# Performance work log

Hardware: AMD Instinct MI355X
Metric: run time of the kernel (lower is better)

## Reference

```python
import jax, jax.numpy as jnp
import numpy as np

NEG = -100000.0
V, E, HID, K = 30000, 256, 512, 32   # vocab, embed_dim, hidden_size, tag_size
H = HID // 2                          # per-direction LSTM hidden
B, T = 128, 512                       # batch, seq_len
START, END = K - 2, K - 1


def setup_inputs() -> dict:
    keys = iter(jax.random.split(jax.random.key(0), 40))

    def u(shape, scale):
        return jax.random.uniform(next(keys), shape, jnp.float32, -scale, scale)

    inp = {}
    inp["words"] = jax.random.randint(next(keys), (B, T), 0, V)
    inp["labels"] = jax.random.randint(next(keys), (B, T), 0, K - 2)
    inp["emb"] = jax.random.normal(next(keys), (V, E), jnp.float32)
    s = 1.0 / float(np.sqrt(H))
    for l, din in [(0, E), (1, HID)]:
        for d in ("f", "b"):
            inp[f"Wih{l}{d}"] = u((4 * H, din), s)
            inp[f"Whh{l}{d}"] = u((4 * H, H), s)
            inp[f"b{l}{d}"] = u((4 * H,), s)
    st = 1.0 / float(np.sqrt(HID))
    inp["Wtag"] = u((K, HID), st)
    inp["btag"] = u((K,), st)
    tm = u((K, K), float(np.sqrt(3.0 / K)))  # kaiming-uniform-like
    inp["trans"] = tm.at[START, :].set(NEG).at[:, END].set(NEG)
    return inp


def _lstm_dir(x, Wih, Whh, b, reverse):
    # x: [T, B, Din] seq-major; standard torch LSTM cell, gate order i,f,g,o
    Hd = Whh.shape[1]
    z = jnp.zeros((x.shape[1], Hd), x.dtype)

    def step(carry, xt):
        h, c = carry
        g = xt @ Wih.T + h @ Whh.T + b
        i, f, gg, o = jnp.split(g, 4, axis=-1)
        c = jax.nn.sigmoid(f) * c + jax.nn.sigmoid(i) * jnp.tanh(gg)
        h = jax.nn.sigmoid(o) * jnp.tanh(c)
        return (h, c), h

    _, hs = jax.lax.scan(step, (z, z), x, reverse=reverse)
    return hs  # [T, B, Hd], aligned with x even when reverse=True


def reference(words, labels, emb, Wih0f, Whh0f, b0f, Wih0b, Whh0b, b0b,
              Wih1f, Whh1f, b1f, Wih1b, Whh1b, b1b, Wtag, btag, trans):
    x = emb[words].transpose(1, 0, 2)  # [T, B, E]
    h1 = jnp.concatenate([_lstm_dir(x, Wih0f, Whh0f, b0f, False),
                          _lstm_dir(x, Wih0b, Whh0b, b0b, True)], axis=-1)
    h2 = jnp.concatenate([_lstm_dir(h1, Wih1f, Whh1f, b1f, False),
                          _lstm_dir(h1, Wih1b, Whh1b, b1b, True)], axis=-1)
    emit = h2 @ Wtag.T + btag          # [T, B, K]
    lab = labels.T                     # [T, B]
    Bn = lab.shape[1]

    # ---- gold path score ----
    prev = jnp.concatenate([jnp.full((1, Bn), START, lab.dtype), lab], axis=0)
    cur = jnp.concatenate([lab, jnp.full((1, Bn), END, lab.dtype)], axis=0)
    gold_trans = trans[cur, prev].sum(axis=0)                                   # [B]
    gold_emit = jnp.take_along_axis(emit, lab[:, :, None], axis=-1)[..., 0].sum(axis=0)
    gold = gold_trans + gold_emit

    # ---- log partition (forward algorithm) ----
    dp0 = jnp.full((Bn, K), NEG, emit.dtype).at[:, START].set(0.0)

    def part_step(dp, e_t):
        cur_logit = trans[None] + e_t[:, :, None] + dp[:, None, :]  # [B, K_cur, K_prev]
        return jax.nn.logsumexp(cur_logit, axis=-1), None

    dp, _ = jax.lax.scan(part_step, dp0, emit)
    logZ = jax.nn.logsumexp(dp + trans[END][None, :], axis=-1)
    nll = jnp.mean(logZ - gold)

    # ---- viterbi (max-plus DP + backtrace) ----
    def vit_step(dp_v, e_t):
        cur_score = trans[None] + e_t[:, :, None] + dp_v[:, None, :]
        return cur_score.max(axis=-1), cur_score.argmax(axis=-1)

    dpv, bps = jax.lax.scan(vit_step, dp0, emit)   # bps: [T, B, K]
    dpv = dpv + trans[END][None, :]
    best = dpv.argmax(axis=-1)                      # [B]

    def back(tag, bp_t):
        prev_tag = jnp.take_along_axis(bp_t, tag[:, None], axis=1)[:, 0]
        return prev_tag, tag

    _, path = jax.lax.scan(back, best, bps, reverse=True)  # [T, B]
    return nll, path.T
```

## Files before the change

### kernel.cpp

```cpp
#include <hip/hip_runtime.h>
#include <math.h>

#define T_LEN 512
#define BATCH 128
#define KTAG  32
#define START_TAG 30
#define END_TAG   31
#define NEGV  -100000.0f

#define L2E    1.4426950408889634f
#define TWOL2E 2.8853900817779268f
#define LN2    0.6931471805599453f

typedef __attribute__((ext_vector_type(4))) short bf16x4;
typedef __attribute__((ext_vector_type(8))) short bf16x8;
typedef __attribute__((ext_vector_type(4))) float f32x4;
#define MFMA16   __builtin_amdgcn_mfma_f32_16x16x32_bf16
#define MFMA16F8 __builtin_amdgcn_mfma_f32_16x16x32_fp8_fp8
#define EXP2(x)  __builtin_amdgcn_exp2f(x)
#define RCP(x)   __builtin_amdgcn_rcpf(x)

__device__ __forceinline__ short f2bf(float x) {
    unsigned int u = __float_as_uint(x);
    u += 0x7fffu + ((u >> 16) & 1u);
    return (short)(u >> 16);
}

__device__ __forceinline__ f32x4 bf4_to_f32x4(bf16x4 v) {
    union { bf16x4 s; uint2 u; } c; c.s = v;
    f32x4 r;
    r[0] = __uint_as_float(c.u.x << 16);
    r[1] = __uint_as_float(c.u.x & 0xffff0000u);
    r[2] = __uint_as_float(c.u.y << 16);
    r[3] = __uint_as_float(c.u.y & 0xffff0000u);
    return r;
}

__device__ __forceinline__ unsigned char f2fp8(float x) {
    unsigned u = __float_as_uint(x);
    unsigned s = (u >> 24) & 0x80u;
    unsigned mag = u & 0x7fffffffu;
    if (mag >= 0x43e80000u) return (unsigned char)(s | 0x7e);
    int e = (int)(mag >> 23) - 127;
    int ulp_exp = (e < -6) ? -9 : (e - 3);
    float C = __uint_as_float((unsigned)((ulp_exp + 23 + 127) << 23)) * 1.5f;
    float r = (__uint_as_float(mag) + C) - C;
    unsigned ru = __float_as_uint(r);
    int re = (int)(ru >> 23) - 127;
    unsigned code;
    if (r == 0.0f) code = 0;
    else if (re < -6) code = (unsigned)(r * 512.0f);
    else code = (unsigned)((re + 7) << 3) | ((ru >> 20) & 7u);
    return (unsigned char)(s | code);
}

__device__ __forceinline__ unsigned pack2_fp8(float h0, float h1) {
#if __has_builtin(__builtin_amdgcn_cvt_pk_fp8_f32)
    return (unsigned)__builtin_amdgcn_cvt_pk_fp8_f32(h0, h1, 0, false);
#else
    return (unsigned)f2fp8(h0) | ((unsigned)f2fp8(h1) << 8);
#endif
}

__global__ void fill_kernel(float* out, int n, float v) {
    int i = blockIdx.x * 256 + threadIdx.x;
    if (i < n) out[i] = v;
}

__device__ __forceinline__ void dev_pack_bf16(const float* __restrict__ W,
                                              short* __restrict__ out, int K, int idx) {
    const int KT = K >> 5;
    int i  = idx & 7;
    int ln = (idx >> 3) & 63;
    int rem = idx >> 9;
    int kt = rem % KT;
    int wt = rem / KT;
    int type = wt & 3, w = wt >> 2;
    int row = type * 256 + w * 16 + (ln & 15);
    int col = kt * 32 + ((ln >> 4) << 3) + i;
    float sc = (type == 2) ? TWOL2E : L2E;
    out[idx] = f2bf(W[(size_t)row * K + col] * sc);
}

__device__ __forceinline__ void dev_pack_fp8(const float* __restrict__ W,
                                             unsigned char* __restrict__ out, int K, int idx) {
    const int KT = K >> 5;
    int i  = idx & 7;
    int ln = (idx >> 3) & 63;
    int rem = idx >> 9;
    int kt = rem % KT;
    int wt = rem / KT;
    int type = wt & 3, w = wt >> 2;
    int row = type * 256 + w * 16 + (ln & 15);
    int col = kt * 32 + ((ln >> 4) << 3) + i;
    float sc = (type == 2) ? TWOL2E : L2E;
    out[idx] = f2fp8(W[(size_t)row * K + col] * sc);
}

__device__ __forceinline__ void dev_pack_wtag(const float* __restrict__ Wtag,
                                              unsigned char* __restrict__ out, int idx) {
    int i  = idx & 7;
    int ln = (idx >> 3) & 63;
    int kt = (idx >> 9) & 7;
    int nt = (idx >> 12) & 1;
    int dir = idx >> 13;
    int row = nt * 16 + (ln & 15);
    int col = dir * 256 + kt * 32 + ((ln >> 4) << 3) + i;
    out[idx] = f2fp8(Wtag[row * 512 + col]);
}

__global__ __launch_bounds__(256) void pack_all(
    const float* Wih0f, const float* Wih0b, const float* Wih1f, const float* Wih1b,
    const float* Whh0f, const float* Whh0b, const float* Whh1f, const float* Whh1b,
    const float* Wtag, const float* emb,
    short* wq0f, short* wq0b, short* wq1f, short* wq1b,
    unsigned char* h80f, unsigned char* h80b, unsigned char* h81f, unsigned char* h81b,
    unsigned char* wtag8, short* embq)
{
    const int bx = blockIdx.x;
    const int tid = threadIdx.x;
    if (bx < 2048) {
        const float* W = (bx < 1024) ? Wih0f : Wih0b;
        short* o = (bx < 1024) ? wq0f : wq0b;
        dev_pack_bf16(W, o, 256, (bx & 1023) * 256 + tid);
    } else if (bx < 6144) {
        const float* W = (bx < 4096) ? Wih1f : Wih1b;
        short* o = (bx < 4096) ? wq1f : wq1b;
        dev_pack_bf16(W, o, 512, ((bx - 2048) & 2047) * 256 + tid);
    } else if (bx < 10240) {
        int seg = (bx - 6144) >> 10;
        const float* W = (seg == 0) ? Whh0f : (seg == 1) ? Whh0b : (seg == 2) ? Whh1f : Whh1b;
        unsigned char* o = (seg == 0) ? h80f : (seg == 1) ? h80b : (seg == 2) ? h81f : h81b;
        dev_pack_fp8(W, o, 256, ((bx - 6144) & 1023) * 256 + tid);
    } else if (bx < 10304) {
        dev_pack_wtag(Wtag, wtag8, (bx - 10240) * 256 + tid);
    } else {
        int i = (bx - 10304) * 256 + tid;
        embq[i] = f2bf(emb[i]);
    }
}

template <int LAYER, int AMODE>
__device__ __forceinline__ void gemm_role(
    int gb, int C, const int* __restrict__ words, const void* __restrict__ Asrc,
    const short* __restrict__ BfF, const short* __restrict__ BfB,
    const float* __restrict__ bsF, const float* __restrict__ bsB,
    short* __restrict__ preF, short* __restrict__ preB, int s0, char* smraw)
{
    constexpr int K  = (LAYER == 0) ? 256 : 512;
    constexpr int KT = K / 32;
    constexpr int RB = K * 2;
    constexpr int NT = (LAYER == 0) ? 2 : 1;
    constexpr int NH = 4 / NT;

    const int dir = gb / (NH * C);
    int rem = gb - dir * NH * C;
    const int half = rem / C;
    const int gx = rem - half * C;
    const int sblk = gx >> 3, bg = gx & 7;
    const int t0 = half * NT;
    const int tid = threadIdx.x;
    const int wv = tid >> 6, L = tid & 63;
    const int wid = wv;
    const int brow = L & 15, kgrp = L >> 4;

    const short* Bf = dir ? BfB : BfF;
    const float* bias = dir ? bsB : bsF;
    short* pre = dir ? preB : preF;
    short* As = (short*)smraw;

    const bf16x8* Bp = (const bf16x8*)Bf;
    bf16x8 bw[NT][KT];
#pragma unroll
    for (int u = 0; u < NT; ++u)
#pragma unroll
        for (int kt = 0; kt < KT; ++kt)
            bw[u][kt] = Bp[(((wid * 4 + t0 + u) * KT + kt) << 6) + L];

    float bb[NT];
#pragma unroll
    for (int u = 0; u < NT; ++u) {
        float sc = ((t0 + u) == 2) ? TWOL2E : L2E;
        bb[u] = bias[(t0 + u) * 256 + wid * 16 + brow] * sc;
    }

    for (int sl = 0; sl < 8; ++sl) {
        const int sloc = sblk * 8 + sl;
        const int t = dir ? (T_LEN - 1 - (s0 + sloc)) : (s0 + sloc);

        {
            char* lds = (char*)As;
            if (LAYER == 0) {
                if (tid < 512) {
                    const int row = tid >> 5, ch = tid & 31;
                    const int b = bg * 16 + row;
                    const int cb = ch * 16;
                    const int word = words[b * T_LEN + t];
                    if (AMODE == 0) {
                        const char* src = (const char*)Asrc + (size_t)word * 512 + cb;
                        *(bf16x8*)(lds + ((row * RB + cb) ^ ((row & 7) << 4))) = *(const bf16x8*)src;
                    } else {
                        const float* src = (const float*)Asrc + (size_t)word * 256 + ch * 8;
                        float4 f0 = *(const float4*)(src);
                        float4 f1 = *(const float4*)(src + 4);
                        short tmp[8] = {f2bf(f0.x), f2bf(f0.y), f2bf(f0.z), f2bf(f0.w),
                                        f2bf(f1.x), f2bf(f1.y), f2bf(f1.z), f2bf(f1.w)};
                        *(bf16x8*)(lds + ((row * RB + cb) ^ ((row & 7) << 4))) = *(const bf16x8*)tmp;
                    }
                }
            } else {
                const int row = tid >> 6, ch = tid & 63;
                const int b = bg * 16 + row;
                const int cb = ch * 16;
                const char* src = (const char*)Asrc + ((size_t)t * BATCH + b) * 1024 + cb;
                *(bf16x8*)(lds + ((row * RB + cb) ^ ((row & 7) << 4))) = *(const bf16x8*)src;
            }
        }
        __syncthreads();

        f32x4 acc[NT];
#pragma unroll
        for (int u = 0; u < NT; ++u) acc[u] = (f32x4){bb[u], bb[u], bb[u], bb[u]};

        const char* lds = (const char*)As;
#pragma unroll
        for (int kt = 0; kt < KT; ++kt) {
            bf16x8 a = *(const bf16x8*)(lds + ((brow * RB + kt * 64 + kgrp * 16) ^ ((brow & 7) << 4)));
#pragma unroll
            for (int u = 0; u < NT; ++u)
                acc[u] = MFMA16(a, bw[u][kt], acc[u], 0, 0, 0);
        }

        bf16x4* pp = (bf16x4*)pre;
        const size_t base = ((((size_t)sloc * 8 + bg) * 16 + wid) * 4 + t0) * 64 + L;
#pragma unroll
        for (int u = 0; u < NT; ++u) {
            bf16x4 o = {f2bf(acc[u][0]), f2bf(acc[u][1]), f2bf(acc[u][2]), f2bf(acc[u][3])};
            pp[base + (size_t)u * 64] = o;
        }
        __syncthreads();
    }
}

__global__ __launch_bounds__(1024) void gemm_only0(
    const int* words, const void* Asrc, const short* BfF, const short* BfB,
    const float* bsF, const float* bsB, short* preF, short* preB, int s0, int C, int amode)
{
    constexpr int SMB = 8192;
    __shared__ __align__(16) char smraw[SMB];
    if (amode == 0)
        gemm_role<0, 0>(blockIdx.x, C, words, Asrc, BfF, BfB, bsF, bsB, preF, preB, s0, smraw);
    else
        gemm_role<0, 1>(blockIdx.x, C, words, Asrc, BfF, BfB, bsF, bsB, preF, preB, s0, smraw);
}

__global__ __launch_bounds__(1024) void gemm_only1(
    const int* words, const void* Asrc, const short* BfF, const short* BfB,
    const float* bsF, const float* bsB, short* preF, short* preB, int s0, int C)
{
    constexpr int SMB = 16384;
    __shared__ __align__(16) char smraw[SMB];
    gemm_role<1, 2>(blockIdx.x, C, words, Asrc, BfF, BfB, bsF, bsB, preF, preB, s0, smraw);
}

template <int LAYER, int AMODE>
__global__ __launch_bounds__(1024) void fused_chunk(
    const int* __restrict__ words, const void* __restrict__ xsrc,
    const short* __restrict__ wihF, const short* __restrict__ wihB,
    const float* __restrict__ biasF, const float* __restrict__ biasB,
    short* __restrict__ preOutF, short* __restrict__ preOutB, int s0g, int gemm_on,
    const short* __restrict__ preF, const short* __restrict__ preB,
    const unsigned char* __restrict__ whhF, const unsigned char* __restrict__ whhB,
    short* __restrict__ h1out,
    const unsigned char* __restrict__ wtagf, const float* __restrict__ btag,
    float* __restrict__ emitF, float* __restrict__ emitB,
    float* __restrict__ stC, long* __restrict__ stH,
    int s0, int C)
{
    constexpr int SMB = (LAYER == 1) ? (8704 + 32768) : 8704;
    __shared__ __align__(16) char smraw[SMB];

    if (blockIdx.x >= 32) {
        if (gemm_on)
            gemm_role<LAYER, AMODE>(blockIdx.x - 32, C, words, xsrc, wihF, wihB,
                                    biasF, biasB, preOutF, preOutB, s0g, smraw);
        return;
    }

    const int dir  = blockIdx.x >> 4;
    const int bg   = (blockIdx.x >> 1) & 7;
    const int half = blockIdx.x & 1;
    const int tid = threadIdx.x;
    const int wid = tid >> 6;
    const int L   = tid & 63;
    const int brow = L & 15;
    const int kgrp = L >> 4;
    const int Lp = (L + half * 32) & 63;

    const bf16x4* pre = (const bf16x4*)(dir ? preB : preF);
    long* hb0 = (long*)smraw;
    long* hb1 = (long*)(smraw + 4352);
    float (*ep)[8][16][32] = (float(*)[8][16][32])(smraw + 8704);

    const long* Wp = (const long*)(dir ? whhB : whhF);
    long whh[32];
#pragma unroll
    for (int tt = 0; tt < 4; ++tt)
#pragma unroll
        for (int kt = 0; kt < 8; ++kt)
            whh[tt * 8 + kt] = Wp[(((wid * 4 + tt) * 8 + kt) << 6) + L];

    long wt0 = 0, wt1 = 0;
    if (LAYER == 1) {
        int kw = (wid < 8) ? wid : 7;
        const long* wtp = (const long*)wtagf;
        wt0 = wtp[(((dir * 2 + 0) * 8 + kw) << 6) + L];
        wt1 = wtp[(((dir * 2 + 1) * 8 + kw) << 6) + L];
    }

    float cs0, cs1;
    if (s0 == 0) {
        for (int q = tid; q < 544; q += 1024) hb0[q] = 0;
        cs0 = cs1 = 0.f;
    } else {
        for (int q = tid; q < 544; q += 1024)
            hb0[q] = stH[(size_t)blockIdx.x * 544 + q];
        float2 c2 = ((const float2*)stC)[blockIdx.x * 1024 + tid];
        cs0 = c2.x; cs1 = c2.y;
    }
    for (int q = tid; q < 544; q += 1024) hb1[q] = 0;
    __syncthreads();

    const size_t pstride = 8 * 16 * 4 * 64;
    const size_t pbase = (((size_t)bg * 16 + wid) * 4) * 64 + Lp;
    bf16x4 pc0 = pre[pbase + 0 * 64];
    bf16x4 pc1 = pre[pbase + 1 * 64];
    bf16x4 pc2 = pre[pbase + 2 * 64];
    bf16x4 pc3 = pre[pbase + 3 * 64];

    const int srcL = L & 31;
    const bool lo = (L < 32);
    const int rb = ((srcL >> 4) << 2) + (lo ? 0 : 2);
    const int jj = wid * 16 + (L & 15);

    for (int s = s0; s < s0 + C; ++s) {
        const int sloc = s - s0;
        const int par = s & 1;
        const char* ldsr = (const char*)(par ? hb1 : hb0);
        char* ldsw = (char*)(par ? hb0 : hb1);

        f32x4 acc0 = bf4_to_f32x4(pc0);
        f32x4 acc1 = bf4_to_f32x4(pc1);
        f32x4 acc2 = bf4_to_f32x4(pc2);
        f32x4 acc3 = bf4_to_f32x4(pc3);

        {
            const int sl2 = (sloc + 1 < C) ? sloc + 1 : sloc;
            const size_t pb = (size_t)sl2 * pstride + pbase;
            pc0 = pre[pb + 0 * 64];
            pc1 = pre[pb + 1 * 64];
            pc2 = pre[pb + 2 * 64];
            pc3 = pre[pb + 3 * 64];
        }

#pragma unroll
        for (int kt = 0; kt < 8; ++kt) {
            long a = *(const long*)(ldsr + brow * 272 + kt * 32 + kgrp * 8);
            acc0 = MFMA16F8(a, whh[0 * 8 + kt], acc0, 0, 0, 0);
            acc1 = MFMA16F8(a, whh[1 * 8 + kt], acc1, 0, 0, 0);
            acc2 = MFMA16F8(a, whh[2 * 8 + kt], acc2, 0, 0, 0);
            acc3 = MFMA16F8(a, whh[3 * 8 + kt], acc3, 0, 0, 0);
        }

        if (LAYER == 1 && sloc >= 1 && wid < 8) {
            long a = *(const long*)(ldsr + brow * 272 + wid * 32 + kgrp * 8);
            f32x4 e0 = {0.f, 0.f, 0.f, 0.f}, e1 = {0.f, 0.f, 0.f, 0.f};
            e0 = MFMA16F8(a, wt0, e0, 0, 0, 0);
            e1 = MFMA16F8(a, wt1, e1, 0, 0, 0);
#pragma unroll
            for (int r = 0; r < 4; ++r) {
                int bl = (kgrp << 2) + r;
                ep[par][wid][bl][brow] = e0[r];
                ep[par][wid][bl][16 + brow] = e1[r];
            }
        }

        if (LAYER == 1 && sloc >= 2 && tid < 256) {
            int bl = tid >> 5, tg = tid & 31;
            float v = 0.f;
#pragma unroll
            for (int p = 0; p < 8; ++p) v += ep[par ^ 1][p][bl][tg];
            const int x = s - 2;
            const int tp = dir ? (T_LEN - 1 - x) : x;
            size_t ei = ((size_t)tp * BATCH + bg * 16 + half * 8 + bl) * KTAG + tg;
            if (dir == 0) emitF[ei] = v + btag[tg];
            else          emitB[ei] = v;
        }

        float g0v0, g0v1, g1v0, g1v1, g2v0, g2v1, g3v0, g3v1;
        {
            float a00 = __shfl(acc0[2], srcL), a01 = __shfl(acc0[3], srcL);
            float a10 = __shfl(acc1[2], srcL), a11 = __shfl(acc1[3], srcL);
            float a20 = __shfl(acc2[2], srcL), a21 = __shfl(acc2[3], srcL);
            float a30 = __shfl(acc3[2], srcL), a31 = __shfl(acc3[3], srcL);
            g0v0 = lo ? acc0[0] : a00;  g0v1 = lo ? acc0[1] : a01;
            g1v0 = lo ? acc1[0] : a10;  g1v1 = lo ? acc1[1] : a11;
            g2v0 = lo ? acc2[0] : a20;  g2v1 = lo ? acc2[1] : a21;
            g3v0 = lo ? acc3[0] : a30;  g3v1 = lo ? acc3[1] : a31;
        }

        float hh0, hh1;
        {
            float ig, fg, gg, og;
            ig = RCP(1.0f + EXP2(-g0v0)); fg = RCP(1.0f + EXP2(-g1v0));
            gg = 1.0f - 2.0f * RCP(1.0f + EXP2(g2v0));
            og = RCP(1.0f + EXP2(-g3v0));
            cs0 = fg * cs0 + ig * gg;
            hh0 = og * (1.0f - 2.0f * RCP(1.0f + EXP2(TWOL2E * cs0)));
            ig = RCP(1.0f + EXP2(-g0v1)); fg = RCP(1.0f + EXP2(-g1v1));
            gg = 1.0f - 2.0f * RCP(1.0f + EXP2(g2v1));
            og = RCP(1.0f + EXP2(-g3v1));
            cs1 = fg * cs1 + ig * gg;
            hh1 = og * (1.0f - 2.0f * RCP(1.0f + EXP2(TWOL2E * cs1)));
        }

        {
            unsigned pk = pack2_fp8(hh0, hh1);
            ldsw[(rb + 0) * 272 + jj] = (char)(pk);
            ldsw[(rb + 1) * 272 + jj] = (char)(pk >> 8);
            if (LAYER == 0) {
                const int t = dir ? (T_LEN - 1 - s) : s;
                size_t gb = ((size_t)t * BATCH + bg * 16 + half * 8 + rb) * 512 + dir * 256 + jj;
                h1out[gb]       = f2bf(hh0);
                h1out[gb + 512] = f2bf(hh1);
            }
        }
        __syncthreads();
    }

    if (LAYER == 1) {
        if (wid < 8) {
            const char* ldsr = (const char*)hb0;
            long a = *(const long*)(ldsr + brow * 272 + wid * 32 + kgrp * 8);
            f32x4 e0 = {0.f, 0.f, 0.f, 0.f}, e1 = {0.f, 0.f, 0.f, 0.f};
            e0 = MFMA16F8(a, wt0, e0, 0, 0, 0);
            e1 = MFMA16F8(a, wt1, e1, 0, 0, 0);
#pragma unroll
            for (int r = 0; r < 4; ++r) {
                int bl = (kgrp << 2) + r;
                ep[0][wid][bl][brow] = e0[r];
                ep[0][wid][bl][16 + brow] = e1[r];
            }
        }
        if (tid < 256) {
            int bl = tid >> 5, tg = tid & 31;
            float v = 0.f;
#pragma unroll
            for (int p = 0; p < 8; ++p) v += ep[1][p][bl][tg];
            const int x = s0 + C - 2;
            const int tp = dir ? (T_LEN - 1 - x) : x;
            size_t ei = ((size_t)tp * BATCH + bg * 16 + half * 8 + bl) * KTAG + tg;
            if (dir == 0) emitF[ei] = v + btag[tg];
            else          emitB[ei] = v;
        }
        __syncthreads();
        if (tid < 256) {
            int bl = tid >> 5, tg = tid & 31;
            float v = 0.f;
#pragma unroll
            for (int p = 0; p < 8; ++p) v += ep[0][p][bl][tg];
            const int x = s0 + C - 1;
            const int tp = dir ? (T_LEN - 1 - x) : x;
            size_t ei = ((size_t)tp * BATCH + bg * 16 + half * 8 + bl) * KTAG + tg;
            if (dir == 0) emitF[ei] = v + btag[tg];
            else          emitB[ei] = v;
        }
    }

    for (int q = tid; q < 544; q += 1024)
        stH[(size_t)blockIdx.x * 544 + q] = hb0[q];
    ((float2*)stC)[blockIdx.x * 1024 + tid] = (float2){cs0, cs1};
}

__global__ __launch_bounds__(64) void crf_half(
    const float* __restrict__ emitF, const float* __restrict__ emitB,
    const float* __restrict__ trans,
    float* __restrict__ alph, float* __restrict__ betap,
    float* __restrict__ alphV, float* __restrict__ betaV,
    unsigned char* __restrict__ bpsW, unsigned char* __restrict__ npsW)
{
    const int lane = threadIdx.x;
    const int k = lane & 31;
    const int h = lane >> 5;
    const int p0 = h << 4;
    const int role = blockIdx.x >> 7;
    const int b = blockIdx.x & 127;

    __shared__ unsigned char ptr_l[256 * KTAG];

    if (role == 0) {
        float trow2[16];
#pragma unroll
        for (int i = 0; i < 4; ++i) {
            float4 f = *(const float4*)(trans + k * KTAG + p0 + i * 4);
            trow2[i * 4 + 0] = f.x * L2E; trow2[i * 4 + 1] = f.y * L2E;
            trow2[i * 4 + 2] = f.z * L2E; trow2[i * 4 + 3] = f.w * L2E;
        }
        float dp = (k == START_TAG) ? 0.0f : NEGV * L2E;
        size_t e0i = (size_t)b * KTAG + k;
        float e2 = (emitF[e0i] + emitB[e0i]) * L2E;

        for (int t = 0; t < 256; ++t) {
            float e_next2 = 0.0f;
            if (t + 1 < 256) {
                size_t ei = ((size_t)(t + 1) * BATCH + b) * KTAG + k;
                e_next2 = (emitF[ei] + emitB[ei]) * L2E;
            }
            float v[16];
#pragma unroll
            for (int q = 0; q < 16; ++q)
                v[q] = trow2[q] + __shfl(dp, p0 + q);
            float mx[8];
#pragma unroll
            for (int i = 0; i < 8; ++i) mx[i] = fmaxf(v[i], v[i + 8]);
#pragma unroll
            for (int i = 0; i < 4; ++i) mx[i] = fmaxf(mx[i], mx[i + 4]);
            float halfm = fmaxf(fmaxf(mx[0], mx[1]), fmaxf(mx[2], mx[3]));
            float m = fmaxf(halfm, __shfl_xor(halfm, 32));
            float es[16];
#pragma unroll
            for (int i = 0; i < 16; ++i) es[i] = EXP2(v[i] - m);
#pragma unroll
            for (int i = 0; i < 8; ++i) es[i] += es[i + 8];
#pragma unroll
            for (int i = 0; i < 4; ++i) es[i] += es[i + 4];
            float shalf = (es[0] + es[1]) + (es[2] + es[3]);
            float ssum = shalf + __shfl_xor(shalf, 32);
            dp = e2 + m + __log2f(ssum);
            e2 = e_next2;
        }
        if (lane < 32) alph[b * KTAG + k] = dp;
    } else if (role == 1) {
        float trowT2[16];
#pragma unroll
        for (int i = 0; i < 16; ++i)
            trowT2[i] = trans[(p0 + i) * KTAG + k] * L2E;
        float beta = trans[END_TAG * KTAG + k] * L2E;
        size_t e0i = ((size_t)511 * BATCH + b) * KTAG + k;
        float e2 = (emitF[e0i] + emitB[e0i]) * L2E;

        for (int it = 0; it < 256; ++it) {
            const int t = 510 - it;
            float e_next2 = 0.0f;
            if (it + 1 < 256) {
                size_t ei = ((size_t)t * BATCH + b) * KTAG + k;
                e_next2 = (emitF[ei] + emitB[ei]) * L2E;
            }
            float z = beta + e2;
            float v[16];
#pragma unroll
            for (int q = 0; q < 16; ++q)
                v[q] = trowT2[q] + __shfl(z, p0 + q);
            float mx[8];
#pragma unroll
            for (int i = 0; i < 8; ++i) mx[i] = fmaxf(v[i], v[i + 8]);
#pragma unroll
            for (int i = 0; i < 4; ++i) mx[i] = fmaxf(mx[i], mx[i + 4]);
            float halfm = fmaxf(fmaxf(mx[0], mx[1]), fmaxf(mx[2], mx[3]));
            float m = fmaxf(halfm, __shfl_xor(halfm, 32));
            float es[16];
#pragma unroll
            for (int i = 0; i < 16; ++i) es[i] = EXP2(v[i] - m);
#pragma unroll
            for (int i = 0; i < 8; ++i) es[i] += es[i + 8];
#pragma unroll
            for (int i = 0; i < 4; ++i) es[i] += es[i + 4];
            float shalf = (es[0] + es[1]) + (es[2] + es[3]);
            float ssum = shalf + __shfl_xor(shalf, 32);
            beta = m + __log2f(ssum);
            e2 = e_next2;
        }
        if (lane < 32) betap[b * KTAG + k] = beta;
    } else if (role == 2) {
        float trow[16];
#pragma unroll
        for (int i = 0; i < 4; ++i) {
            float4 f = *(const float4*)(trans + k * KTAG + p0 + i * 4);
            trow[i * 4 + 0] = f.x; trow[i * 4 + 1] = f.y;
            trow[i * 4 + 2] = f.z; trow[i * 4 + 3] = f.w;
        }
        float dpv = (k == START_TAG) ? 0.0f : NEGV;
        size_t e0i = (size_t)b * KTAG + k;
        float e = emitF[e0i] + emitB[e0i];

        for (int t = 0; t < 256; ++t) {
            float e_next = 0.0f;
            if (t + 1 < 256) {
                size_t ei = ((size_t)(t + 1) * BATCH + b) * KTAG + k;
                e_next = emitF[ei] + emitB[ei];
            }
            float w[16];
#pragma unroll
            for (int q = 0; q < 16; ++q)
                w[q] = trow[q] + __shfl(dpv, p0 + q);
            float bv_[8]; int bi_[8];
#pragma unroll
            for (int i = 0; i < 8; ++i) {
                bool g = w[2 * i + 1] > w[2 * i];
                bv_[i] = g ? w[2 * i + 1] : w[2 * i];
                bi_[i] = p0 + (g ? 2 * i + 1 : 2 * i);
            }
#pragma unroll
            for (int i = 0; i < 4; ++i) {
                bool g = bv_[2 * i + 1] > bv_[2 * i];
                bv_[i] = g ? bv_[2 * i + 1] : bv_[2 * i];
                bi_[i] = g ? bi_[2 * i + 1] : bi_[2 * i];
            }
            { bool g = bv_[3] > bv_[2]; bv_[1] = g ? bv_[3] : bv_[2]; bi_[1] = g ? bi_[3] : bi_[2]; }
            { bool g = bv_[1] > bv_[0]; bv_[0] = g ? bv_[1] : bv_[0]; bi_[0] = g ? bi_[1] : bi_[0]; }
            float ov = __shfl_xor(bv_[0], 32);
            int   oi = __shfl_xor(bi_[0], 32);
            bool g2 = h ? (ov >= bv_[0]) : (ov > bv_[0]);
            float bm  = g2 ? ov : bv_[0];
            int  barg = g2 ? oi : bi_[0];
            dpv = e + bm;
            if (!h) ptr_l[t * KTAG + k] = (unsigned char)barg;
            e = e_next;
        }
        if (lane < 32) alphV[b * KTAG + k] = dpv;
        for (int i = lane; i < 2048; i += 64)
            ((unsigned*)bpsW)[(size_t)b * 2048 + i] = ((const unsigned*)ptr_l)[i];
    } else {
        float trowT[16];
#pragma unroll
        for (int i = 0; i < 16; ++i)
            trowT[i] = trans[(p0 + i) * KTAG + k];
        float bvv = trans[END_TAG * KTAG + k];
        size_t e0i = ((size_t)511 * BATCH + b) * KTAG + k;
        float e = emitF[e0i] + emitB[e0i];

        for (int it = 0; it < 256; ++it) {
            const int t = 510 - it;
            float e_next = 0.0f;
            if (it + 1 < 256) {
                size_t ei = ((size_t)t * BATCH + b) * KTAG + k;
                e_next = emitF[ei] + emitB[ei];
            }
            float z = bvv + e;
            float w[16];
#pragma unroll
            for (int q = 0; q < 16; ++q)
                w[q] = trowT[q] + __shfl(z, p0 + q);
            float bv_[8]; int bi_[8];
#pragma unroll
            for (int i = 0; i < 8; ++i) {
                bool g = w[2 * i + 1] > w[2 * i];
                bv_[i] = g ? w[2 * i + 1] : w[2 * i];
                bi_[i] = p0 + (g ? 2 * i + 1 : 2 * i);
            }
#pragma unroll
            for (int i = 0; i < 4; ++i) {
                bool g = bv_[2 * i + 1] > bv_[2 * i];
                bv_[i] = g ? bv_[2 * i + 1] : bv_[2 * i];
                bi_[i] = g ? bi_[2 * i + 1] : bi_[2 * i];
            }
            { bool g = bv_[3] > bv_[2]; bv_[1] = g ? bv_[3] : bv_[2]; bi_[1] = g ? bi_[3] : bi_[2]; }
            { bool g = bv_[1] > bv_[0]; bv_[0] = g ? bv_[1] : bv_[0]; bi_[0] = g ? bi_[1] : bi_[0]; }
            float ov = __shfl_xor(bv_[0], 32);
            int   oi = __shfl_xor(bi_[0], 32);
            bool g2 = h ? (ov >= bv_[0]) : (ov > bv_[0]);
            float bm  = g2 ? ov : bv_[0];
            int  barg = g2 ? oi : bi_[0];
            bvv = bm;
            if (!h) ptr_l[(t - 255) * KTAG + k] = (unsigned char)barg;
            e = e_next;
        }
        if (lane < 32) betaV[b * KTAG + k] = bvv;
        for (int i = lane; i < 2048; i += 64)
            ((unsigned*)npsW)[(size_t)b * 2048 + i] = ((const unsigned*)ptr_l)[i];
    }
}

__global__ __launch_bounds__(64) void crf_join(
    const float* __restrict__ emitF, const float* __restrict__ emitB,
    const float* __restrict__ trans, const int* __restrict__ labels,
    const float* __restrict__ alph, const float* __restrict__ betap,
    const float* __restrict__ alphV, const float* __restrict__ betaV,
    const unsigned char* __restrict__ bpsW, const unsigned char* __restrict__ npsW,
    float* __restrict__ diff, float* __restrict__ path_out)
{
    const int b = blockIdx.x;
    const int lane = threadIdx.x;
    const int k = lane & 31;

    __shared__ unsigned char bps_l[256 * KTAG];
    __shared__ unsigned char nps_l[256 * KTAG];
    __shared__ unsigned char pth[T_LEN];

    for (int i = lane; i < 2048; i += 64) {
        ((unsigned*)bps_l)[i] = ((const unsigned*)bpsW)[(size_t)b * 2048 + i];
        ((unsigned*)nps_l)[i] = ((const unsigned*)npsW)[(size_t)b * 2048 + i];
    }

    float fv = alph[b * KTAG + k] + betap[b * KTAG + k];
    float mm = fv;
    for (int off = 16; off; off >>= 1) mm = fmaxf(mm, __shfl_xor(mm, off));
    float contrib = (lane < KTAG) ? EXP2(fv - mm) : 0.0f;
    float ss = contrib;
    for (int off = 32; off; off >>= 1) ss += __shfl_xor(ss, off);
    float logZ = (mm + __log2f(ss)) * LN2;

    float gsum = 0.0f;
    for (int t = lane; t < T_LEN; t += 64) {
        int curl = labels[b * T_LEN + t];
        int prev = (t > 0) ? labels[b * T_LEN + t - 1] : START_TAG;
        size_t gi = ((size_t)t * BATCH + b) * KTAG + curl;
        gsum += trans[curl * KTAG + prev] + emitF[gi] + emitB[gi];
    }
    if (lane == 0) gsum += trans[END_TAG * KTAG + labels[b * T_LEN + T_LEN - 1]];
    for (int off = 32; off; off >>= 1) gsum += __shfl_xor(gsum, off);

    float av = alphV[b * KTAG + k] + betaV[b * KTAG + k];
    int bi = k;
    for (int off = 16; off; off >>= 1) {
        float ovv = __shfl_xor(av, off);
        int   oii = __shfl_xor(bi, off);
        if (ovv > av || (ovv == av && oii < bi)) { av = ovv; bi = oii; }
    }

    __syncthreads();
    if (lane == 0) {
        diff[b] = logZ - gsum;
        int pb = bi, pf = bi;
        pth[255] = (unsigned char)bi;
        for (int i = 1; i <= 256; ++i) {
            if (i <= 255) {
                pb = bps_l[(256 - i) * KTAG + pb];
                pth[255 - i] = (unsigned char)pb;
            }
            pf = nps_l[(i - 1) * KTAG + pf];
            pth[255 + i] = (unsigned char)pf;
        }
    }
    __syncthreads();
    for (int t = lane; t < T_LEN; t += 64)
        path_out[(size_t)b * T_LEN + t] = (float)pth[t];
}

__global__ void nll_kernel(const float* __restrict__ diff, float* __restrict__ out) {
    int lane = threadIdx.x;
    float v = diff[lane];
    __shared__ float red[2];
    for (int off = 32; off; off >>= 1) v += __shfl_xor(v, off);
    if ((lane & 63) == 0) red[lane >> 6] = v;
    __syncthreads();
    if (lane == 0) out[0] = (red[0] + red[1]) / 128.0f;
}

extern "C" void kernel_launch(void* const* d_in, const int* in_sizes, int n_in,
                              void* d_out, int out_size, void* d_ws, size_t ws_size,
                              hipStream_t stream) {
    (void)in_sizes; (void)n_in;

    const int*   words  = (const int*)d_in[0];
    const int*   labels = (const int*)d_in[1];
    const float* emb    = (const float*)d_in[2];
    const float* Wih0f  = (const float*)d_in[3];
    const float* Whh0f  = (const float*)d_in[4];
    const float* b0f    = (const float*)d_in[5];
    const float* Wih0b  = (const float*)d_in[6];
    const float* Whh0b  = (const float*)d_in[7];
    const float* b0b    = (const float*)d_in[8];
    const float* Wih1f  = (const float*)d_in[9];
    const float* Whh1f  = (const float*)d_in[10];
    const float* b1f    = (const float*)d_in[11];
    const float* Wih1b  = (const float*)d_in[12];
    const float* Whh1b  = (const float*)d_in[13];
    const float* b1b    = (const float*)d_in[14];
    const float* Wtag   = (const float*)d_in[15];
    const float* btag   = (const float*)d_in[16];
    const float* trans  = (const float*)d_in[17];
    float* out = (float*)d_out;
    char* ws = (char*)d_ws;

    const size_t WIH0B = (size_t)1024 * 256 * 2;
    const size_t WIH1B = (size_t)1024 * 512 * 2;
    const size_t WHH8B = (size_t)1024 * 256;
    const size_t WTAG8 = (size_t)16384;
    const size_t H1B   = (size_t)T_LEN * BATCH * 512 * 2;
    const size_t EMITB = (size_t)T_LEN * BATCH * KTAG * 4;
    const size_t EMBQB = (size_t)30000 * 256 * 2;
    const size_t STHB  = (size_t)32 * 544 * 8;
    const size_t STCB  = (size_t)32 * 1024 * 8;
    const size_t PSTEP = (size_t)BATCH * 1024 * 2;
    const size_t CRFAB = (size_t)4 * 128 * 32 * 4;
    const size_t BPSB  = (size_t)128 * 256 * 32;

    const size_t base0 = 2 * WIH0B + 2 * WIH1B + 4 * WHH8B + WTAG8 + H1B +
                         2 * EMITB + STHB + STCB + CRFAB + 2 * BPSB +
                         4096 + (1u << 20);

    int C = 0, use_embq = 0;
    for (int eq = 1; eq >= 0 && !C; --eq)
        for (int c = 256; c >= 16 && !C; c >>= 1)
            if (base0 + (eq ? EMBQB : 0) + 4 * (size_t)c * PSTEP <= ws_size) {
                C = c; use_embq = eq;
            }
    if (!C) {
        fill_kernel<<<(out_size + 255) / 256, 256, 0, stream>>>(
            out, out_size, (float)(ws_size >> 20));
        return;
    }

    size_t off = 0;
    auto alloc = [&](size_t bytes) -> char* {
        char* p = ws + off;
        off = (off + bytes + 255) & ~(size_t)255;
        return p;
    };
    short* wihq0f = (short*)alloc(WIH0B);
    short* wihq0b = (short*)alloc(WIH0B);
    short* wihq1f = (short*)alloc(WIH1B);
    short* wihq1b = (short*)alloc(WIH1B);
    unsigned char* whh8_0f = (unsigned char*)alloc(WHH8B);
    unsigned char* whh8_0b = (unsigned char*)alloc(WHH8B);
    unsigned char* whh8_1f = (unsigned char*)alloc(WHH8B);
    unsigned char* whh8_1b = (unsigned char*)alloc(WHH8B);
    unsigned char* wtag8   = (unsigned char*)alloc(WTAG8);
    short* h1     = (short*)alloc(H1B);
    float* emF    = (float*)alloc(EMITB);
    float* emB    = (float*)alloc(EMITB);
    long*  stH    = (long*)alloc(STHB);
    float* stC    = (float*)alloc(STCB);
    float* diff   = (float*)alloc(4096);
    float* crfa   = (float*)alloc(CRFAB);
    unsigned char* bpsW = (unsigned char*)alloc(BPSB);
    unsigned char* npsW = (unsigned char*)alloc(BPSB);
    short* preFb[2], * preBb[2];
    preFb[0] = (short*)alloc((size_t)C * PSTEP);
    preFb[1] = (short*)alloc((size_t)C * PSTEP);
    preBb[0] = (short*)alloc((size_t)C * PSTEP);
    preBb[1] = (short*)alloc((size_t)C * PSTEP);
    short* embq = use_embq ? (short*)alloc(EMBQB) : nullptr;

    float* alph  = crfa;
    float* betap = crfa + 128 * 32;
    float* alphV = crfa + 2 * 128 * 32;
    float* betaV = crfa + 3 * 128 * 32;

    {
        int nblk = 10304 + (use_embq ? 30000 : 0);
        pack_all<<<nblk, 256, 0, stream>>>(
            Wih0f, Wih0b, Wih1f, Wih1b, Whh0f, Whh0b, Whh1f, Whh1b, Wtag, emb,
            wihq0f, wihq0b, wihq1f, wihq1b,
            whh8_0f, whh8_0b, whh8_1f, whh8_1b, wtag8, embq);
    }

    const int NC = T_LEN / C;
    const void* xsrc0 = use_embq ? (const void*)embq : (const void*)emb;
    const int am = use_embq ? 0 : 1;

    gemm_only0<<<4 * C, 1024, 0, stream>>>(words, xsrc0, wihq0f, wihq0b,
                                           b0f, b0b, preFb[0], preBb[0], 0, C, am);
    for (int c = 0; c < NC; ++c) {
        int on = (c + 1 < NC);
        if (use_embq)
            fused_chunk<0, 0><<<32 + 4 * C, 1024, 0, stream>>>(
                words, xsrc0, wihq0f, wihq0b, b0f, b0b,
                preFb[(c + 1) & 1], preBb[(c + 1) & 1], (c + 1) * C, on,
                preFb[c & 1], preBb[c & 1], whh8_0f, whh8_0b, h1,
                wtag8, btag, emF, emB, stC, stH, c * C, C);
        else
            fused_chunk<0, 1><<<32 + 4 * C, 1024, 0, stream>>>(
                words, xsrc0, wihq0f, wihq0b, b0f, b0b,
                preFb[(c + 1) & 1], preBb[(c + 1) & 1], (c + 1) * C, on,
                preFb[c & 1], preBb[c & 1], whh8_0f, whh8_0b, h1,
                wtag8, btag, emF, emB, stC, stH, c * C, C);
    }
    gemm_only1<<<8 * C, 1024, 0, stream>>>(nullptr, h1, wihq1f, wihq1b,
                                           b1f, b1b, preFb[0], preBb[0], 0, C);
    for (int c = 0; c < NC; ++c) {
        int on = (c + 1 < NC);
        fused_chunk<1, 2><<<32 + 8 * C, 1024, 0, stream>>>(
            nullptr, h1, wihq1f, wihq1b, b1f, b1b,
            preFb[(c + 1) & 1], preBb[(c + 1) & 1], (c + 1) * C, on,
            preFb[c & 1], preBb[c & 1], whh8_1f, whh8_1b, nullptr,
            wtag8, btag, emF, emB, stC, stH, c * C, C);
    }

    crf_half<<<512, 64, 0, stream>>>(emF, emB, trans,
                                     alph, betap, alphV, betaV, bpsW, npsW);
    crf_join<<<128, 64, 0, stream>>>(emF, emB, trans, labels,
                                     alph, betap, alphV, betaV, bpsW, npsW,
                                     diff, out + 1);
    nll_kernel<<<1, 128, 0, stream>>>(diff, out);
}
```

Measured before the change: 1.758 ms.

## Quantize layer-1 input weights and layer-0 hidden outputs to fp8 for projection GEMM

Packs the layer-1 input-projection weights to fp8 and writes the layer-0 hidden states as fp8 bytes instead of bf16. The layer-1 input GEMM then uses the fp8 MFMA, with half-size LDS rows. Each block now computes two gate tiles instead of one, so half as many GEMM blocks are launched. This halves the h1 memory traffic and the weight footprint, at the cost of lower precision in the second layer's input projection.

```diff
diff --git a/kernel.cpp b/kernel.cpp
--- a/kernel.cpp
+++ b/kernel.cpp
@@ -113,7 +113,7 @@
     const float* Wih0f, const float* Wih0b, const float* Wih1f, const float* Wih1b,
     const float* Whh0f, const float* Whh0b, const float* Whh1f, const float* Whh1b,
     const float* Wtag, const float* emb,
-    short* wq0f, short* wq0b, short* wq1f, short* wq1b,
+    short* wq0f, short* wq0b, unsigned char* wq1f8, unsigned char* wq1b8,
     unsigned char* h80f, unsigned char* h80b, unsigned char* h81f, unsigned char* h81b,
     unsigned char* wtag8, short* embq)
 {
@@ -125,8 +125,8 @@
         dev_pack_bf16(W, o, 256, (bx & 1023) * 256 + tid);
     } else if (bx < 6144) {
         const float* W = (bx < 4096) ? Wih1f : Wih1b;
-        short* o = (bx < 4096) ? wq1f : wq1b;
-        dev_pack_bf16(W, o, 512, ((bx - 2048) & 2047) * 256 + tid);
+        unsigned char* o = (bx < 4096) ? wq1f8 : wq1b8;
+        dev_pack_fp8(W, o, 512, ((bx - 2048) & 2047) * 256 + tid);
     } else if (bx < 10240) {
         int seg = (bx - 6144) >> 10;
         const float* W = (seg == 0) ? Whh0f : (seg == 1) ? Whh0b : (seg == 2) ? Whh1f : Whh1b;
@@ -143,15 +143,15 @@
 template <int LAYER, int AMODE>
 __device__ __forceinline__ void gemm_role(
     int gb, int C, const int* __restrict__ words, const void* __restrict__ Asrc,
-    const short* __restrict__ BfF, const short* __restrict__ BfB,
+    const void* __restrict__ BfF, const void* __restrict__ BfB,
     const float* __restrict__ bsF, const float* __restrict__ bsB,
     short* __restrict__ preF, short* __restrict__ preB, int s0, char* smraw)
 {
     constexpr int K  = (LAYER == 0) ? 256 : 512;
     constexpr int KT = K / 32;
-    constexpr int RB = K * 2;
-    constexpr int NT = (LAYER == 0) ? 2 : 1;
-    constexpr int NH = 4 / NT;
+    constexpr int RB = (LAYER == 0) ? K * 2 : K;
+    constexpr int NT = 2;
+    constexpr int NH = 2;
 
     const int dir = gb / (NH * C);
     int rem = gb - dir * NH * C;
@@ -164,18 +164,28 @@
     const int wid = wv;
     const int brow = L & 15, kgrp = L >> 4;
 
-    const short* Bf = dir ? BfB : BfF;
+    const void* Bf = dir ? BfB : BfF;
     const float* bias = dir ? bsB : bsF;
     short* pre = dir ? preB : preF;
-    short* As = (short*)smraw;
-
-    const bf16x8* Bp = (const bf16x8*)Bf;
-    bf16x8 bw[NT][KT];
-#pragma unroll
-    for (int u = 0; u < NT; ++u)
-#pragma unroll
-        for (int kt = 0; kt < KT; ++kt)
-            bw[u][kt] = Bp[(((wid * 4 + t0 + u) * KT + kt) << 6) + L];
+    char* lds = smraw;
+
+    bf16x8 bw16[LAYER == 0 ? NT * KT : 1][1];
+    long   bw8[LAYER == 1 ? NT * KT : 1];
+    if (LAYER == 0) {
+        const bf16x8* Bp = (const bf16x8*)Bf;
+#pragma unroll
+        for (int u = 0; u < NT; ++u)
+#pragma unroll
+            for (int kt = 0; kt < KT; ++kt)
+                bw16[u * KT + kt][0] = Bp[(((wid * 4 + t0 + u) * KT + kt) << 6) + L];
+    } else {
+        const long* Bp = (const long*)Bf;
+#pragma unroll
+        for (int u = 0; u < NT; ++u)
+#pragma unroll
+            for (int kt = 0; kt < KT; ++kt)
+                bw8[u * KT + kt] = Bp[(((wid * 4 + t0 + u) * KT + kt) << 6) + L];
+    }
 
     float bb[NT];
 #pragma unroll
@@ -188,33 +198,31 @@
         const int sloc = sblk * 8 + sl;
         const int t = dir ? (T_LEN - 1 - (s0 + sloc)) : (s0 + sloc);
 
-        {
-            char* lds = (char*)As;
-            if (LAYER == 0) {
-                if (tid < 512) {
-                    const int row = tid >> 5, ch = tid & 31;
-                    const int b = bg * 16 + row;
-                    const int cb = ch * 16;
-                    const int word = words[b * T_LEN + t];
-                    if (AMODE == 0) {
-                        const char* src = (const char*)Asrc + (size_t)word * 512 + cb;
-                        *(bf16x8*)(lds + ((row * RB + cb) ^ ((row & 7) << 4))) = *(const bf16x8*)src;
-                    } else {
-                        const float* src = (const float*)Asrc + (size_t)word * 256 + ch * 8;
-                        float4 f0 = *(const float4*)(src);
-                        float4 f1 = *(const float4*)(src + 4);
-                        short tmp[8] = {f2bf(f0.x), f2bf(f0.y), f2bf(f0.z), f2bf(f0.w),
-                                        f2bf(f1.x), f2bf(f1.y), f2bf(f1.z), f2bf(f1.w)};
-                        *(bf16x8*)(lds + ((row * RB + cb) ^ ((row & 7) << 4))) = *(const bf16x8*)tmp;
-                    }
-                }
-            } else {
-                const int row = tid >> 6, ch = tid & 63;
+        if (LAYER == 0) {
+            if (tid < 512) {
+                const int row = tid >> 5, ch = tid & 31;
                 const int b = bg * 16 + row;
                 const int cb = ch * 16;
-                const char* src = (const char*)Asrc + ((size_t)t * BATCH + b) * 1024 + cb;
-                *(bf16x8*)(lds + ((row * RB + cb) ^ ((row & 7) << 4))) = *(const bf16x8*)src;
-            }
+                const int word = words[b * T_LEN + t];
+                if (AMODE == 0) {
+                    const char* src = (const char*)Asrc + (size_t)word * 512 + cb;
+                    *(bf16x8*)(lds + ((row * RB + cb) ^ ((row & 7) << 4))) = *(const bf16x8*)src;
+                } else {
+                    const float* src = (const float*)Asrc + (size_t)word * 256 + ch * 8;
+                    float4 f0 = *(const float4*)(src);
+                    float4 f1 = *(const float4*)(src + 4);
+                    short tmp[8] = {f2bf(f0.x), f2bf(f0.y), f2bf(f0.z), f2bf(f0.w),
+                                    f2bf(f1.x), f2bf(f1.y), f2bf(f1.z), f2bf(f1.w)};
+                    *(bf16x8*)(lds + ((row * RB + cb) ^ ((row & 7) << 4))) = *(const bf16x8*)tmp;
+                }
+            }
+        } else {
+            const int row = tid >> 6, ch = tid & 63;
+            const int b = bg * 16 + row;
+            const int cb = ch * 8;
+            const unsigned char* src = (const unsigned char*)Asrc +
+                                       ((size_t)t * BATCH + b) * 512 + cb;
+            *(long*)(lds + ((row * RB + cb) ^ ((row & 7) << 3))) = *(const long*)src;
         }
         __syncthreads();
 
@@ -222,13 +230,19 @@
 #pragma unroll
         for (int u = 0; u < NT; ++u) acc[u] = (f32x4){bb[u], bb[u], bb[u], bb[u]};
 
-        const char* lds = (const char*)As;
 #pragma unroll
         for (int kt = 0; kt < KT; ++kt) {
-            bf16x8 a = *(const bf16x8*)(lds + ((brow * RB + kt * 64 + kgrp * 16) ^ ((brow & 7) << 4)));
-#pragma unroll
-            for (int u = 0; u < NT; ++u)
-                acc[u] = MFMA16(a, bw[u][kt], acc[u], 0, 0, 0);
+            if (LAYER == 0) {
+                bf16x8 a = *(const bf16x8*)(lds + ((brow * RB + kt * 64 + kgrp * 16) ^ ((brow & 7) << 4)));
+#pragma unroll
+                for (int u = 0; u < NT; ++u)
+                    acc[u] = MFMA16(a, bw16[u * KT + kt][0], acc[u], 0, 0, 0);
+            } else {
+                long a = *(const long*)(lds + ((brow * RB + kt * 32 + kgrp * 8) ^ ((brow & 7) << 3)));
+#pragma unroll
+                for (int u = 0; u < NT; ++u)
+                    acc[u] = MFMA16F8(a, bw8[u * KT + kt], acc[u], 0, 0, 0);
+            }
         }
 
         bf16x4* pp = (bf16x4*)pre;
@@ -243,11 +257,10 @@
 }
 
 __global__ __launch_bounds__(1024) void gemm_only0(
-    const int* words, const void* Asrc, const short* BfF, const short* BfB,
+    const int* words, const void* Asrc, const void* BfF, const void* BfB,
     const float* bsF, const float* bsB, short* preF, short* preB, int s0, int C, int amode)
 {
-    constexpr int SMB = 8192;
-    __shared__ __align__(16) char smraw[SMB];
+    __shared__ __align__(16) char smraw[8192];
     if (amode == 0)
         gemm_role<0, 0>(blockIdx.x, C, words, Asrc, BfF, BfB, bsF, bsB, preF, preB, s0, smraw);
     else
@@ -255,23 +268,22 @@
 }
 
 __global__ __launch_bounds__(1024) void gemm_only1(
-    const int* words, const void* Asrc, const short* BfF, const short* BfB,
+    const int* words, const void* Asrc, const void* BfF, const void* BfB,
     const float* bsF, const float* bsB, short* preF, short* preB, int s0, int C)
 {
-    constexpr int SMB = 16384;
-    __shared__ __align__(16) char smraw[SMB];
+    __shared__ __align__(16) char smraw[8192];
     gemm_role<1, 2>(blockIdx.x, C, words, Asrc, BfF, BfB, bsF, bsB, preF, preB, s0, smraw);
 }
 
 template <int LAYER, int AMODE>
 __global__ __launch_bounds__(1024) void fused_chunk(
     const int* __restrict__ words, const void* __restrict__ xsrc,
-    const short* __restrict__ wihF, const short* __restrict__ wihB,
+    const void* __restrict__ wihF, const void* __restrict__ wihB,
     const float* __restrict__ biasF, const float* __restrict__ biasB,
     short* __restrict__ preOutF, short* __restrict__ preOutB, int s0g, int gemm_on,
     const short* __restrict__ preF, const short* __restrict__ preB,
     const unsigned char* __restrict__ whhF, const unsigned char* __restrict__ whhB,
-    short* __restrict__ h1out,
+    unsigned char* __restrict__ h1out,
     const unsigned char* __restrict__ wtagf, const float* __restrict__ btag,
     float* __restrict__ emitF, float* __restrict__ emitB,
     float* __restrict__ stC, long* __restrict__ stH,
@@ -431,8 +443,8 @@
             if (LAYER == 0) {
                 const int t = dir ? (T_LEN - 1 - s) : s;
                 size_t gb = ((size_t)t * BATCH + bg * 16 + half * 8 + rb) * 512 + dir * 256 + jj;
-                h1out[gb]       = f2bf(hh0);
-                h1out[gb + 512] = f2bf(hh1);
+                h1out[gb]       = (unsigned char)pk;
+                h1out[gb + 512] = (unsigned char)(pk >> 8);
             }
         }
         __syncthreads();
@@ -784,10 +796,10 @@
     char* ws = (char*)d_ws;
 
     const size_t WIH0B = (size_t)1024 * 256 * 2;
-    const size_t WIH1B = (size_t)1024 * 512 * 2;
+    const size_t WIH1B = (size_t)1024 * 512;
     const size_t WHH8B = (size_t)1024 * 256;
     const size_t WTAG8 = (size_t)16384;
-    const size_t H1B   = (size_t)T_LEN * BATCH * 512 * 2;
+    const size_t H1B   = (size_t)T_LEN * BATCH * 512;
     const size_t EMITB = (size_t)T_LEN * BATCH * KTAG * 4;
     const size_t EMBQB = (size_t)30000 * 256 * 2;
     const size_t STHB  = (size_t)32 * 544 * 8;
@@ -820,14 +832,14 @@
     };
     short* wihq0f = (short*)alloc(WIH0B);
     short* wihq0b = (short*)alloc(WIH0B);
-    short* wihq1f = (short*)alloc(WIH1B);
-    short* wihq1b = (short*)alloc(WIH1B);
+    unsigned char* wihq1f8 = (unsigned char*)alloc(WIH1B);
+    unsigned char* wihq1b8 = (unsigned char*)alloc(WIH1B);
     unsigned char* whh8_0f = (unsigned char*)alloc(WHH8B);
     unsigned char* whh8_0b = (unsigned char*)alloc(WHH8B);
     unsigned char* whh8_1f = (unsigned char*)alloc(WHH8B);
     unsigned char* whh8_1b = (unsigned char*)alloc(WHH8B);
     unsigned char* wtag8   = (unsigned char*)alloc(WTAG8);
-    short* h1     = (short*)alloc(H1B);
+    unsigned char* h1      = (unsigned char*)alloc(H1B);
     float* emF    = (float*)alloc(EMITB);
     float* emB    = (float*)alloc(EMITB);
     long*  stH    = (long*)alloc(STHB);
@@ -852,7 +864,7 @@
         int nblk = 10304 + (use_embq ? 30000 : 0);
         pack_all<<<nblk, 256, 0, stream>>>(
             Wih0f, Wih0b, Wih1f, Wih1b, Whh0f, Whh0b, Whh1f, Whh1b, Wtag, emb,
-            wihq0f, wihq0b, wihq1f, wihq1b,
+            wihq0f, wihq0b, wihq1f8, wihq1b8,
             whh8_0f, whh8_0b, whh8_1f, whh8_1b, wtag8, embq);
     }
 
@@ -877,12 +889,12 @@
                 preFb[c & 1], preBb[c & 1], whh8_0f, whh8_0b, h1,
                 wtag8, btag, emF, emB, stC, stH, c * C, C);
     }
-    gemm_only1<<<8 * C, 1024, 0, stream>>>(nullptr, h1, wihq1f, wihq1b,
+    gemm_only1<<<4 * C, 1024, 0, stream>>>(nullptr, h1, wihq1f8, wihq1b8,
                                            b1f, b1b, preFb[0], preBb[0], 0, C);
     for (int c = 0; c < NC; ++c) {
         int on = (c + 1 < NC);
-        fused_chunk<1, 2><<<32 + 8 * C, 1024, 0, stream>>>(
-            nullptr, h1, wihq1f, wihq1b, b1f, b1b,
+        fused_chunk<1, 2><<<32 + 4 * C, 1024, 0, stream>>>(
+            nullptr, h1, wihq1f8, wihq1b8, b1f, b1b,
             preFb[(c + 1) & 1], preBb[(c + 1) & 1], (c + 1) * C, on,
             preFb[c & 1], preBb[c & 1], whh8_1f, whh8_1b, nullptr,
             wtag8, btag, emF, emB, stC, stH, c * C, C);
```

New measurement: 1.738 ms. No clear change (-1.1%).
